# Kernel optimization log

Measured on AMD Instinct MI355X. Metric: run time of the kernel, lower is better.

Reference implementation:

```python
import jax, jax.numpy as jnp
import numpy as np

N_NODES = 65536
N_EDGES = 1048576
IN_FEATS = 128
H1 = 128
H2 = 256
N_CLASSES = 16


def setup_inputs() -> dict:
    key = jax.random.key(0)
    ks = jax.random.split(key, 12)
    s = 0.05
    x = jax.random.normal(ks[0], (N_NODES, IN_FEATS), dtype=jnp.float32)
    src = jax.random.randint(ks[1], (N_EDGES,), 0, N_NODES, dtype=jnp.int32)
    dst = jax.random.randint(ks[2], (N_EDGES,), 0, N_NODES, dtype=jnp.int32)
    # SAGEConv('pool') params: fc_pool (bias), fc_self (no bias), fc_neigh (no bias), output bias
    Wp = jax.random.normal(ks[3], (H1, IN_FEATS), dtype=jnp.float32) * s
    bp = jnp.zeros((H1,), dtype=jnp.float32)
    Ws = jax.random.normal(ks[4], (H1, IN_FEATS), dtype=jnp.float32) * s
    Wn = jax.random.normal(ks[5], (H1, H1), dtype=jnp.float32) * s
    bn = jnp.zeros((H1,), dtype=jnp.float32)
    # MLP head
    W1 = jax.random.normal(ks[6], (H2, H1), dtype=jnp.float32) * s
    b1 = jnp.zeros((H2,), dtype=jnp.float32)
    W2 = jax.random.normal(ks[7], (N_CLASSES, H2), dtype=jnp.float32) * s
    b2 = jnp.zeros((N_CLASSES,), dtype=jnp.float32)
    return {"x": x, "Wp": Wp, "bp": bp, "Ws": Ws, "Wn": Wn, "bn": bn,
            "W1": W1, "b1": b1, "W2": W2, "b2": b2, "src": src, "dst": dst}


def reference(x, Wp, bp, Ws, Wn, bn, W1, b1, W2, b2, src, dst):
    N = x.shape[0]
    # SAGEConv 'pool': per-edge MLP on gathered source features, segment-max over dst
    m = jax.nn.relu(x[src] @ Wp.T + bp)              # [E, H1]
    pooled = jax.ops.segment_max(m, dst, num_segments=N)  # [N, H1], -inf for isolated
    pooled = jnp.where(jnp.isneginf(pooled), 0.0, pooled)
    h = x @ Ws.T + pooled @ Wn.T + bn                # combine self + neigh
    h = jax.nn.leaky_relu(h)                         # slope 0.01 matches torch default
    h = jax.nn.leaky_relu(h @ W1.T + b1)
    # dropout is identity in eval mode
    h = jax.nn.sigmoid(h @ W2.T + b2)
    return h
```

## Files before the change

### kernel.cpp

```cpp
#include <hip/hip_runtime.h>
#include <cstdint>
#include <cstddef>

typedef __attribute__((ext_vector_type(8))) __bf16 bf16x8;
typedef __attribute__((ext_vector_type(4))) float f32x4;

union bf8pack { unsigned short u[8]; bf16x8 v; uint4 q; };

static __device__ __forceinline__ unsigned short f2b(float f) {
    union { float f; unsigned int u; } v; v.f = f;
    unsigned int u = v.u;
    unsigned int r = (u + 0x7fffu + ((u >> 16) & 1u)) >> 16;
    return (unsigned short)r;
}

template<int K, int ACT>
__global__ __launch_bounds__(256) void mfma_gemm(
    const unsigned short* __restrict__ A, int strideA,
    const unsigned short* __restrict__ W,
    const float* __restrict__ bias,
    unsigned short* __restrict__ C, int Ncols)
{
    const int nt = Ncols >> 7;
    const int bm = (int)blockIdx.x / nt, bn = (int)blockIdx.x % nt;
    const int w  = threadIdx.x >> 6;
    const int wm = w & 1, wn = w >> 1;
    const int l  = threadIdx.x & 63;
    const int lr = l & 15, quad = l >> 4;
    const int m0 = bm * 128 + wm * 64;
    const int n0 = bn * 128 + wn * 64;

    f32x4 acc[4][4];
#pragma unroll
    for (int i = 0; i < 4; i++)
#pragma unroll
        for (int j = 0; j < 4; j++) acc[i][j] = (f32x4){0.f, 0.f, 0.f, 0.f};

    const unsigned short* Ap = A + (size_t)(m0 + lr) * strideA + quad * 8;
    const unsigned short* Bp = W + (size_t)(n0 + lr) * K + quad * 8;

    for (int ks = 0; ks < K / 32; ks++) {
        bf16x8 af[4], bf[4];
#pragma unroll
        for (int i = 0; i < 4; i++)
            af[i] = *(const bf16x8*)(Ap + (size_t)i * 16 * strideA + ks * 32);
#pragma unroll
        for (int i = 0; i < 4; i++)
            bf[i] = *(const bf16x8*)(Bp + (size_t)i * 16 * K + ks * 32);
#pragma unroll
        for (int mi = 0; mi < 4; mi++)
#pragma unroll
            for (int ni = 0; ni < 4; ni++)
                acc[mi][ni] = __builtin_amdgcn_mfma_f32_16x16x32_bf16(
                    af[mi], bf[ni], acc[mi][ni], 0, 0, 0);
    }

#pragma unroll
    for (int ni = 0; ni < 4; ni++) {
        const int col = n0 + ni * 16 + lr;
        const float bv = bias[col];
#pragma unroll
        for (int mi = 0; mi < 4; mi++) {
#pragma unroll
            for (int r = 0; r < 4; r++) {
                const int row = m0 + mi * 16 + quad * 4 + r;
                float v = acc[mi][ni][r] + bv;
                if (ACT == 1) v = v > 0.f ? v : 0.f;
                if (ACT == 2) v = v > 0.f ? v : 0.01f * v;
                C[(size_t)row * Ncols + col] = f2b(v);
            }
        }
    }
}

__global__ __launch_bounds__(256) void k1_fused(
    const float* __restrict__ x, const unsigned short* __restrict__ Wp_b,
    const float* __restrict__ bias, unsigned short* __restrict__ bufX,
    unsigned short* __restrict__ y)
{
    const int bm = blockIdx.x;
    const int w  = threadIdx.x >> 6;
    const int wm = w & 1, wn = w >> 1;
    const int l  = threadIdx.x & 63;
    const int lr = l & 15, quad = l >> 4;
    const int m0 = bm * 128 + wm * 64;
    const int n0 = wn * 64;

    f32x4 acc[4][4];
#pragma unroll
    for (int i = 0; i < 4; i++)
#pragma unroll
        for (int j = 0; j < 4; j++) acc[i][j] = (f32x4){0.f, 0.f, 0.f, 0.f};

    const float* Ap = x + (size_t)(m0 + lr) * 128 + quad * 8;
    const unsigned short* Bp = Wp_b + (size_t)(n0 + lr) * 128 + quad * 8;

#pragma unroll
    for (int ks = 0; ks < 4; ks++) {
        bf16x8 af[4], bf[4];
#pragma unroll
        for (int i = 0; i < 4; i++) {
            const float* p = Ap + (size_t)i * 16 * 128 + ks * 32;
            float4 f0 = *(const float4*)p;
            float4 f1 = *(const float4*)(p + 4);
            bf8pack pk;
            pk.u[0] = f2b(f0.x); pk.u[1] = f2b(f0.y);
            pk.u[2] = f2b(f0.z); pk.u[3] = f2b(f0.w);
            pk.u[4] = f2b(f1.x); pk.u[5] = f2b(f1.y);
            pk.u[6] = f2b(f1.z); pk.u[7] = f2b(f1.w);
            af[i] = pk.v;
            if (wn == 0)
                *(uint4*)(bufX + (size_t)(m0 + lr + i * 16) * 256 + ks * 32 + quad * 8) = pk.q;
        }
#pragma unroll
        for (int i = 0; i < 4; i++)
            bf[i] = *(const bf16x8*)(Bp + (size_t)i * 16 * 128 + ks * 32);
#pragma unroll
        for (int mi = 0; mi < 4; mi++)
#pragma unroll
            for (int ni = 0; ni < 4; ni++)
                acc[mi][ni] = __builtin_amdgcn_mfma_f32_16x16x32_bf16(
                    af[mi], bf[ni], acc[mi][ni], 0, 0, 0);
    }

#pragma unroll
    for (int ni = 0; ni < 4; ni++) {
        const int col = n0 + ni * 16 + lr;
        const float bv = bias[col];
#pragma unroll
        for (int mi = 0; mi < 4; mi++) {
#pragma unroll
            for (int r = 0; r < 4; r++) {
                const int row = m0 + mi * 16 + quad * 4 + r;
                float v = acc[mi][ni][r] + bv;
                v = v > 0.f ? v : 0.f;
                y[(size_t)row * 128 + col] = f2b(v);
            }
        }
    }
}

__global__ __launch_bounds__(256) void head_mfma(
    const unsigned short* __restrict__ H, const unsigned short* __restrict__ W2b,
    const float* __restrict__ b2, float* __restrict__ out)
{
    const int wave = (int)(blockIdx.x * 4) + (threadIdx.x >> 6);
    const int l = threadIdx.x & 63;
    const int lr = l & 15, quad = l >> 4;
    const int m0 = wave * 16;
    f32x4 acc = (f32x4){0.f, 0.f, 0.f, 0.f};
#pragma unroll
    for (int ks = 0; ks < 8; ks++) {
        bf16x8 a = *(const bf16x8*)(H + (size_t)(m0 + lr) * 256 + ks * 32 + quad * 8);
        bf16x8 b = *(const bf16x8*)(W2b + (size_t)lr * 256 + ks * 32 + quad * 8);
        acc = __builtin_amdgcn_mfma_f32_16x16x32_bf16(a, b, acc, 0, 0, 0);
    }
    const float bv = b2[lr];
#pragma unroll
    for (int r = 0; r < 4; r++) {
        const int row = m0 + quad * 4 + r;
        float v = acc[r] + bv;
        out[(size_t)row * 16 + lr] = 1.f / (1.f + __expf(-v));
    }
}

__global__ __launch_bounds__(256) void count_conv(
    const int* __restrict__ dst, int* __restrict__ bcnt, int E, int ebks,
    const float* __restrict__ Wp, const float* __restrict__ Ws,
    const float* __restrict__ Wn, const float* __restrict__ W1,
    const float* __restrict__ W2,
    unsigned short* __restrict__ Wp_b, unsigned short* __restrict__ Wcat,
    unsigned short* __restrict__ W1_b, unsigned short* __restrict__ W2_b)
{
    if ((int)blockIdx.x >= ebks) {
        int i = ((int)blockIdx.x - ebks) * 256 + threadIdx.x;
        if (i < 16384) {
            Wp_b[i] = f2b(Wp[i]);
        } else if (i < 49152) {
            int j = i - 16384; int o = j >> 8, k = j & 255;
            Wcat[j] = f2b(k < 128 ? Ws[o * 128 + k] : Wn[o * 128 + (k - 128)]);
        } else if (i < 81920) {
            W1_b[i - 49152] = f2b(W1[i - 49152]);
        } else if (i < 86016) {
            W2_b[i - 81920] = f2b(W2[i - 81920]);
        }
        return;
    }
    __shared__ int h[2048];
    for (int i = threadIdx.x; i < 2048; i += 256) h[i] = 0;
    __syncthreads();
    int base = blockIdx.x * 4096;
#pragma unroll
    for (int i = 0; i < 16; i++) {
        int e = base + i * 256 + threadIdx.x;
        if (e < E) atomicAdd(&h[((unsigned)dst[e]) >> 5], 1);
    }
    __syncthreads();
    for (int i = threadIdx.x; i < 2048; i += 256)
        if (h[i]) atomicAdd(&bcnt[i], h[i]);
}

__global__ __launch_bounds__(1024) void bucket_scan(
    const int* __restrict__ bcnt, int* __restrict__ boff, int* __restrict__ bcur)
{
    __shared__ int s[1024];
    int t = threadIdx.x;
    int c0 = bcnt[2 * t], c1 = bcnt[2 * t + 1];
    s[t] = c0 + c1;
    __syncthreads();
    for (int d = 1; d < 1024; d <<= 1) {
        int add = (t >= d) ? s[t - d] : 0;
        __syncthreads();
        s[t] += add;
        __syncthreads();
    }
    int ex = (t == 0) ? 0 : s[t - 1];
    boff[2 * t] = ex;          bcur[2 * t] = ex;
    boff[2 * t + 1] = ex + c0; bcur[2 * t + 1] = ex + c0;
    if (t == 1023) boff[2048] = s[1023];
}

__global__ __launch_bounds__(256) void bucket_scatter(
    const int* __restrict__ src, const int* __restrict__ dst,
    int* __restrict__ bcur, unsigned int* __restrict__ pairs, int E)
{
    __shared__ int h[2048];
    __shared__ int base_l[2048];
    __shared__ int cnt[2048];
    for (int i = threadIdx.x; i < 2048; i += 256) { h[i] = 0; cnt[i] = 0; }
    __syncthreads();
    int base = blockIdx.x * 4096;
    int d_r[16], s_r[16];
#pragma unroll
    for (int i = 0; i < 16; i++) {
        int e = base + i * 256 + threadIdx.x;
        if (e < E) {
            d_r[i] = dst[e]; s_r[i] = src[e];
            atomicAdd(&h[((unsigned)d_r[i]) >> 5], 1);
        } else d_r[i] = -1;
    }
    __syncthreads();
    for (int i = threadIdx.x; i < 2048; i += 256)
        base_l[i] = h[i] ? atomicAdd(&bcur[i], h[i]) : 0;
    __syncthreads();
#pragma unroll
    for (int i = 0; i < 16; i++) {
        if (d_r[i] >= 0) {
            int b = ((unsigned)d_r[i]) >> 5;
            int pos = base_l[b] + atomicAdd(&cnt[b], 1);
            pairs[pos] = ((unsigned)s_r[i] << 5) | ((unsigned)d_r[i] & 31u);
        }
    }
}

__global__ __launch_bounds__(256) void bucket_pool3(
    const unsigned int* __restrict__ yu, const int* __restrict__ boff,
    const unsigned int* __restrict__ pairs, unsigned short* __restrict__ bufX)
{
    __shared__ unsigned short ldsSrc[2048];
    __shared__ int bin[32], offl[32], cnt2[32];
    const int b = blockIdx.x;
    const int tid = threadIdx.x;
    if (tid < 32) { bin[tid] = 0; cnt2[tid] = 0; }
    __syncthreads();
    const int beg = boff[b];
    const int nb = boff[b + 1] - beg;

    for (int i = tid; i < nb; i += 256)
        atomicAdd(&bin[pairs[beg + i] & 31u], 1);
    __syncthreads();
    if (tid == 0) {
        int run = 0;
        for (int i = 0; i < 32; i++) { offl[i] = run; run += bin[i]; }
    }
    __syncthreads();
    for (int i = tid; i < nb; i += 256) {
        unsigned int p = pairs[beg + i];
        int d = p & 31u;
        int slot = offl[d] + atomicAdd(&cnt2[d], 1);
        ldsSrc[slot] = (unsigned short)(p >> 5);
    }
    __syncthreads();

    const int w = tid >> 6, lane = tid & 63;
    for (int ni = 0; ni < 8; ni++) {
        const int n = w * 8 + ni;
        const int e0 = offl[n], cnt = bin[n];
        float ax = 0.f, ay = 0.f;
        for (int e = 0; e < cnt; e += 8) {
            int s[8]; unsigned int v[8];
#pragma unroll
            for (int j = 0; j < 8; j++) {
                int idx = e + j; idx = idx < cnt ? idx : cnt - 1;
                s[j] = ldsSrc[e0 + idx];
            }
#pragma unroll
            for (int j = 0; j < 8; j++) v[j] = yu[(size_t)s[j] * 64 + lane];
#pragma unroll
            for (int j = 0; j < 8; j++) {
                ax = fmaxf(ax, __uint_as_float(v[j] << 16));
                ay = fmaxf(ay, __uint_as_float(v[j] & 0xffff0000u));
            }
        }
        unsigned int packed = (__float_as_uint(ax) >> 16) | (__float_as_uint(ay) & 0xffff0000u);
        ((unsigned int*)bufX)[(size_t)(b * 32 + n) * 128 + 64 + lane] = packed;
    }
}

extern "C" void kernel_launch(void* const* d_in, const int* in_sizes, int n_in,
                              void* d_out, int out_size, void* d_ws, size_t ws_size,
                              hipStream_t stream)
{
    const float* x  = (const float*)d_in[0];
    const float* Wp = (const float*)d_in[1];
    const float* bp = (const float*)d_in[2];
    const float* Ws = (const float*)d_in[3];
    const float* Wn = (const float*)d_in[4];
    const float* bn = (const float*)d_in[5];
    const float* W1 = (const float*)d_in[6];
    const float* b1 = (const float*)d_in[7];
    const float* W2 = (const float*)d_in[8];
    const float* b2 = (const float*)d_in[9];
    const int* src  = (const int*)d_in[10];
    const int* dst  = (const int*)d_in[11];
    float* out = (float*)d_out;

    const int N = in_sizes[0] / 128;
    const int E = in_sizes[10];

    unsigned short* bufX = (unsigned short*)d_ws;
    unsigned short* y    = (unsigned short*)((char*)d_ws + (size_t)32 * 1024 * 1024);
    unsigned short* hbuf = (unsigned short*)((char*)d_ws + (size_t)48 * 1024 * 1024);
    unsigned short* h2   = (unsigned short*)((char*)d_ws + (size_t)64 * 1024 * 1024);

    unsigned short* Wp_b = (unsigned short*)((char*)d_ws + (size_t)96 * 1024 * 1024);
    unsigned short* Wcat = Wp_b + 16384;
    unsigned short* W1_b = Wcat + 32768;
    unsigned short* W2_b = W1_b + 32768;
    int* bcnt = (int*)(W2_b + 4096);
    int* boff = bcnt + 2048;
    int* bcur = boff + 2049 + 3;
    unsigned int* pairs = (unsigned int*)(bcur + 2048);

    dim3 blk(256);
    const int ebks = (E + 4095) / 4096;
    const int cbks = (86016 + 255) / 256;

    hipMemsetAsync(bcnt, 0, 2048 * sizeof(int), stream);
    count_conv<<<ebks + cbks, blk, 0, stream>>>(
        dst, bcnt, E, ebks, Wp, Ws, Wn, W1, W2, Wp_b, Wcat, W1_b, W2_b);
    bucket_scan<<<1, 1024, 0, stream>>>(bcnt, boff, bcur);
    bucket_scatter<<<ebks, blk, 0, stream>>>(src, dst, bcur, pairs, E);

    k1_fused<<<N / 128, blk, 0, stream>>>(x, Wp_b, bp, bufX, y);

    bucket_pool3<<<2048, blk, 0, stream>>>((const unsigned int*)y, boff, pairs, bufX);

    mfma_gemm<256, 2><<<(N / 128) * 1, blk, 0, stream>>>(
        bufX, 256, Wcat, bn, hbuf, 128);

    mfma_gemm<128, 2><<<(N / 128) * 2, blk, 0, stream>>>(
        hbuf, 128, W1_b, b1, h2, 256);

    head_mfma<<<N / 64, blk, 0, stream>>>(h2, W2_b, b2, out);
}
```

Measured before the change: 243.1 us.

## Fuse all GNN stages into one cooperative persistent kernel with grid syncs

Replaces the chain of separate kernel launches (count, scan, scatter, pool, GEMMs, head) with a single cooperative persistent kernel that loops over work items and separates stages with grid.sync. It also overlaps the dst histogram and weight conversion with the first pool-MLP GEMM using an atomic tile cursor, and converts Wp to bf16 inline instead of precomputing it. The goal is to cut per-launch overhead and inter-kernel gaps. In exchange it adds grid-wide barriers, caps the grid at 512 blocks, and hardcodes the problem sizes, dropping the edge-count bounds checks. A multi-kernel fallback is kept for when the cooperative launch fails.

```diff
diff --git a/kernel.cpp b/kernel.cpp
--- a/kernel.cpp
+++ b/kernel.cpp
@@ -1,6 +1,9 @@
 #include <hip/hip_runtime.h>
+#include <hip/hip_cooperative_groups.h>
 #include <cstdint>
 #include <cstddef>
+
+namespace cg = cooperative_groups;
 
 typedef __attribute__((ext_vector_type(8))) __bf16 bf16x8;
 typedef __attribute__((ext_vector_type(4))) float f32x4;
@@ -14,21 +17,17 @@
     return (unsigned short)r;
 }
 
+
 template<int K, int ACT>
-__global__ __launch_bounds__(256) void mfma_gemm(
+static __device__ __forceinline__ void gemm_tile(
     const unsigned short* __restrict__ A, int strideA,
-    const unsigned short* __restrict__ W,
-    const float* __restrict__ bias,
-    unsigned short* __restrict__ C, int Ncols)
-{
-    const int nt = Ncols >> 7;
-    const int bm = (int)blockIdx.x / nt, bn = (int)blockIdx.x % nt;
-    const int w  = threadIdx.x >> 6;
-    const int wm = w & 1, wn = w >> 1;
-    const int l  = threadIdx.x & 63;
-    const int lr = l & 15, quad = l >> 4;
+    const unsigned short* __restrict__ W, const float* __restrict__ bias,
+    unsigned short* __restrict__ C, int Ncols, int bm, int bnt, int tid)
+{
+    const int w = tid >> 6, wm = w & 1, wn = w >> 1;
+    const int l = tid & 63, lr = l & 15, quad = l >> 4;
     const int m0 = bm * 128 + wm * 64;
-    const int n0 = bn * 128 + wn * 64;
+    const int n0 = bnt * 128 + wn * 64;
 
     f32x4 acc[4][4];
 #pragma unroll
@@ -39,20 +38,21 @@
     const unsigned short* Ap = A + (size_t)(m0 + lr) * strideA + quad * 8;
     const unsigned short* Bp = W + (size_t)(n0 + lr) * K + quad * 8;
 
+#pragma unroll
     for (int ks = 0; ks < K / 32; ks++) {
-        bf16x8 af[4], bf[4];
+        bf16x8 af[4], bfr[4];
 #pragma unroll
         for (int i = 0; i < 4; i++)
             af[i] = *(const bf16x8*)(Ap + (size_t)i * 16 * strideA + ks * 32);
 #pragma unroll
         for (int i = 0; i < 4; i++)
-            bf[i] = *(const bf16x8*)(Bp + (size_t)i * 16 * K + ks * 32);
+            bfr[i] = *(const bf16x8*)(Bp + (size_t)i * 16 * K + ks * 32);
 #pragma unroll
         for (int mi = 0; mi < 4; mi++)
 #pragma unroll
             for (int ni = 0; ni < 4; ni++)
                 acc[mi][ni] = __builtin_amdgcn_mfma_f32_16x16x32_bf16(
-                    af[mi], bf[ni], acc[mi][ni], 0, 0, 0);
+                    af[mi], bfr[ni], acc[mi][ni], 0, 0, 0);
     }
 
 #pragma unroll
@@ -73,16 +73,13 @@
     }
 }
 
-__global__ __launch_bounds__(256) void k1_fused(
-    const float* __restrict__ x, const unsigned short* __restrict__ Wp_b,
-    const float* __restrict__ bias, unsigned short* __restrict__ bufX,
-    unsigned short* __restrict__ y)
-{
-    const int bm = blockIdx.x;
-    const int w  = threadIdx.x >> 6;
-    const int wm = w & 1, wn = w >> 1;
-    const int l  = threadIdx.x & 63;
-    const int lr = l & 15, quad = l >> 4;
+static __device__ __forceinline__ void k1_tile(
+    int bm, const float* __restrict__ x, const float* __restrict__ Wp,
+    const float* __restrict__ bp, unsigned short* __restrict__ bufX,
+    unsigned short* __restrict__ yb, int tid)
+{
+    const int w = tid >> 6, wm = w & 1, wn = w >> 1;
+    const int l = tid & 63, lr = l & 15, quad = l >> 4;
     const int m0 = bm * 128 + wm * 64;
     const int n0 = wn * 64;
 
@@ -93,16 +90,15 @@
         for (int j = 0; j < 4; j++) acc[i][j] = (f32x4){0.f, 0.f, 0.f, 0.f};
 
     const float* Ap = x + (size_t)(m0 + lr) * 128 + quad * 8;
-    const unsigned short* Bp = Wp_b + (size_t)(n0 + lr) * 128 + quad * 8;
+    const float* Bp = Wp + (size_t)(n0 + lr) * 128 + quad * 8;
 
 #pragma unroll
     for (int ks = 0; ks < 4; ks++) {
-        bf16x8 af[4], bf[4];
+        bf16x8 af[4], bfr[4];
 #pragma unroll
         for (int i = 0; i < 4; i++) {
             const float* p = Ap + (size_t)i * 16 * 128 + ks * 32;
-            float4 f0 = *(const float4*)p;
-            float4 f1 = *(const float4*)(p + 4);
+            float4 f0 = *(const float4*)p, f1 = *(const float4*)(p + 4);
             bf8pack pk;
             pk.u[0] = f2b(f0.x); pk.u[1] = f2b(f0.y);
             pk.u[2] = f2b(f0.z); pk.u[3] = f2b(f0.w);
@@ -113,20 +109,28 @@
                 *(uint4*)(bufX + (size_t)(m0 + lr + i * 16) * 256 + ks * 32 + quad * 8) = pk.q;
         }
 #pragma unroll
-        for (int i = 0; i < 4; i++)
-            bf[i] = *(const bf16x8*)(Bp + (size_t)i * 16 * 128 + ks * 32);
+        for (int i = 0; i < 4; i++) {
+            const float* p = Bp + (size_t)i * 16 * 128 + ks * 32;
+            float4 f0 = *(const float4*)p, f1 = *(const float4*)(p + 4);
+            bf8pack pk;
+            pk.u[0] = f2b(f0.x); pk.u[1] = f2b(f0.y);
+            pk.u[2] = f2b(f0.z); pk.u[3] = f2b(f0.w);
+            pk.u[4] = f2b(f1.x); pk.u[5] = f2b(f1.y);
+            pk.u[6] = f2b(f1.z); pk.u[7] = f2b(f1.w);
+            bfr[i] = pk.v;
+        }
 #pragma unroll
         for (int mi = 0; mi < 4; mi++)
 #pragma unroll
             for (int ni = 0; ni < 4; ni++)
                 acc[mi][ni] = __builtin_amdgcn_mfma_f32_16x16x32_bf16(
-                    af[mi], bf[ni], acc[mi][ni], 0, 0, 0);
+                    af[mi], bfr[ni], acc[mi][ni], 0, 0, 0);
     }
 
 #pragma unroll
     for (int ni = 0; ni < 4; ni++) {
         const int col = n0 + ni * 16 + lr;
-        const float bv = bias[col];
+        const float bv = bp[col];
 #pragma unroll
         for (int mi = 0; mi < 4; mi++) {
 #pragma unroll
@@ -134,137 +138,110 @@
                 const int row = m0 + mi * 16 + quad * 4 + r;
                 float v = acc[mi][ni][r] + bv;
                 v = v > 0.f ? v : 0.f;
-                y[(size_t)row * 128 + col] = f2b(v);
+                yb[(size_t)row * 128 + col] = f2b(v);
             }
         }
     }
 }
 
-__global__ __launch_bounds__(256) void head_mfma(
-    const unsigned short* __restrict__ H, const unsigned short* __restrict__ W2b,
-    const float* __restrict__ b2, float* __restrict__ out)
-{
-    const int wave = (int)(blockIdx.x * 4) + (threadIdx.x >> 6);
-    const int l = threadIdx.x & 63;
-    const int lr = l & 15, quad = l >> 4;
-    const int m0 = wave * 16;
-    f32x4 acc = (f32x4){0.f, 0.f, 0.f, 0.f};
-#pragma unroll
-    for (int ks = 0; ks < 8; ks++) {
-        bf16x8 a = *(const bf16x8*)(H + (size_t)(m0 + lr) * 256 + ks * 32 + quad * 8);
-        bf16x8 b = *(const bf16x8*)(W2b + (size_t)lr * 256 + ks * 32 + quad * 8);
-        acc = __builtin_amdgcn_mfma_f32_16x16x32_bf16(a, b, acc, 0, 0, 0);
-    }
-    const float bv = b2[lr];
-#pragma unroll
-    for (int r = 0; r < 4; r++) {
-        const int row = m0 + quad * 4 + r;
-        float v = acc[r] + bv;
-        out[(size_t)row * 16 + lr] = 1.f / (1.f + __expf(-v));
-    }
-}
-
-__global__ __launch_bounds__(256) void count_conv(
-    const int* __restrict__ dst, int* __restrict__ bcnt, int E, int ebks,
-    const float* __restrict__ Wp, const float* __restrict__ Ws,
-    const float* __restrict__ Wn, const float* __restrict__ W1,
-    const float* __restrict__ W2,
-    unsigned short* __restrict__ Wp_b, unsigned short* __restrict__ Wcat,
-    unsigned short* __restrict__ W1_b, unsigned short* __restrict__ W2_b)
-{
-    if ((int)blockIdx.x >= ebks) {
-        int i = ((int)blockIdx.x - ebks) * 256 + threadIdx.x;
-        if (i < 16384) {
-            Wp_b[i] = f2b(Wp[i]);
-        } else if (i < 49152) {
-            int j = i - 16384; int o = j >> 8, k = j & 255;
-            Wcat[j] = f2b(k < 128 ? Ws[o * 128 + k] : Wn[o * 128 + (k - 128)]);
-        } else if (i < 81920) {
-            W1_b[i - 49152] = f2b(W1[i - 49152]);
-        } else if (i < 86016) {
-            W2_b[i - 81920] = f2b(W2[i - 81920]);
-        }
-        return;
-    }
-    __shared__ int h[2048];
-    for (int i = threadIdx.x; i < 2048; i += 256) h[i] = 0;
-    __syncthreads();
-    int base = blockIdx.x * 4096;
+static __device__ __forceinline__ void count_chunk(
+    int c, const int* __restrict__ dst, int* __restrict__ bcnt,
+    int* smem, int tid)
+{
+    int* h = smem;
+    for (int i = tid; i < 2048; i += 256) h[i] = 0;
+    __syncthreads();
+    const int base = c * 8192;
+#pragma unroll
+    for (int i = 0; i < 32; i++)
+        atomicAdd(&h[((unsigned)dst[base + i * 256 + tid]) >> 5], 1);
+    __syncthreads();
+    for (int i = tid; i < 2048; i += 256)
+        if (h[i]) atomicAdd(&bcnt[i], h[i]);
+    __syncthreads();
+}
+
+static __device__ __forceinline__ void convw_chunk(
+    int c, const float* __restrict__ Ws, const float* __restrict__ Wn,
+    const float* __restrict__ W1, const float* __restrict__ W2,
+    unsigned short* __restrict__ Wcat, unsigned short* __restrict__ W1_b,
+    unsigned short* __restrict__ W2_b, int tid)
+{
+    int i = c * 16384 + tid;
+    for (int k = 0; k < 64; k++, i += 256) {
+        if (i < 32768) {
+            int o = i >> 8, kk = i & 255;
+            Wcat[i] = f2b(kk < 128 ? Ws[o * 128 + kk] : Wn[o * 128 + (kk - 128)]);
+        } else if (i < 65536) {
+            W1_b[i - 32768] = f2b(W1[i - 32768]);
+        } else if (i < 69632) {
+            W2_b[i - 65536] = f2b(W2[i - 65536]);
+        }
+    }
+}
+
+static __device__ __forceinline__ void scan2048(
+    const int* __restrict__ bcnt, int* __restrict__ boff,
+    int* __restrict__ bcur, int* smem, int tid)
+{
+    int loc[8]; const int base = tid * 8; int s = 0;
+#pragma unroll
+    for (int j = 0; j < 8; j++) { loc[j] = bcnt[base + j]; s += loc[j]; }
+    smem[tid] = s;
+    __syncthreads();
+    for (int d = 1; d < 256; d <<= 1) {
+        int add = (tid >= d) ? smem[tid - d] : 0;
+        __syncthreads();
+        smem[tid] += add;
+        __syncthreads();
+    }
+    int run = tid ? smem[tid - 1] : 0;
+#pragma unroll
+    for (int j = 0; j < 8; j++) { boff[base + j] = run; bcur[base + j] = run; run += loc[j]; }
+    if (tid == 255) boff[2048] = run;
+    __syncthreads();
+}
+
+static __device__ __forceinline__ void scatter_chunk(
+    int c, const int* __restrict__ src, const int* __restrict__ dst,
+    int* __restrict__ bcur, unsigned int* __restrict__ pairs,
+    int* smem, int tid)
+{
+    int* h = smem; int* base_l = smem + 2048; int* cntl = smem + 4096;
+    for (int i = tid; i < 2048; i += 256) { h[i] = 0; cntl[i] = 0; }
+    __syncthreads();
+    const int base = c * 4096;
+    int d_r[16], s_r[16];
 #pragma unroll
     for (int i = 0; i < 16; i++) {
-        int e = base + i * 256 + threadIdx.x;
-        if (e < E) atomicAdd(&h[((unsigned)dst[e]) >> 5], 1);
-    }
-    __syncthreads();
-    for (int i = threadIdx.x; i < 2048; i += 256)
-        if (h[i]) atomicAdd(&bcnt[i], h[i]);
-}
-
-__global__ __launch_bounds__(1024) void bucket_scan(
-    const int* __restrict__ bcnt, int* __restrict__ boff, int* __restrict__ bcur)
-{
-    __shared__ int s[1024];
-    int t = threadIdx.x;
-    int c0 = bcnt[2 * t], c1 = bcnt[2 * t + 1];
-    s[t] = c0 + c1;
-    __syncthreads();
-    for (int d = 1; d < 1024; d <<= 1) {
-        int add = (t >= d) ? s[t - d] : 0;
-        __syncthreads();
-        s[t] += add;
-        __syncthreads();
-    }
-    int ex = (t == 0) ? 0 : s[t - 1];
-    boff[2 * t] = ex;          bcur[2 * t] = ex;
-    boff[2 * t + 1] = ex + c0; bcur[2 * t + 1] = ex + c0;
-    if (t == 1023) boff[2048] = s[1023];
-}
-
-__global__ __launch_bounds__(256) void bucket_scatter(
-    const int* __restrict__ src, const int* __restrict__ dst,
-    int* __restrict__ bcur, unsigned int* __restrict__ pairs, int E)
-{
-    __shared__ int h[2048];
-    __shared__ int base_l[2048];
-    __shared__ int cnt[2048];
-    for (int i = threadIdx.x; i < 2048; i += 256) { h[i] = 0; cnt[i] = 0; }
-    __syncthreads();
-    int base = blockIdx.x * 4096;
-    int d_r[16], s_r[16];
+        int e = base + i * 256 + tid;
+        d_r[i] = dst[e]; s_r[i] = src[e];
+        atomicAdd(&h[((unsigned)d_r[i]) >> 5], 1);
+    }
+    __syncthreads();
+    for (int i = tid; i < 2048; i += 256)
+        base_l[i] = h[i] ? atomicAdd(&bcur[i], h[i]) : 0;
+    __syncthreads();
 #pragma unroll
     for (int i = 0; i < 16; i++) {
-        int e = base + i * 256 + threadIdx.x;
-        if (e < E) {
-            d_r[i] = dst[e]; s_r[i] = src[e];
-            atomicAdd(&h[((unsigned)d_r[i]) >> 5], 1);
-        } else d_r[i] = -1;
-    }
-    __syncthreads();
-    for (int i = threadIdx.x; i < 2048; i += 256)
-        base_l[i] = h[i] ? atomicAdd(&bcur[i], h[i]) : 0;
-    __syncthreads();
-#pragma unroll
-    for (int i = 0; i < 16; i++) {
-        if (d_r[i] >= 0) {
-            int b = ((unsigned)d_r[i]) >> 5;
-            int pos = base_l[b] + atomicAdd(&cnt[b], 1);
-            pairs[pos] = ((unsigned)s_r[i] << 5) | ((unsigned)d_r[i] & 31u);
-        }
-    }
-}
-
-__global__ __launch_bounds__(256) void bucket_pool3(
-    const unsigned int* __restrict__ yu, const int* __restrict__ boff,
-    const unsigned int* __restrict__ pairs, unsigned short* __restrict__ bufX)
-{
-    __shared__ unsigned short ldsSrc[2048];
-    __shared__ int bin[32], offl[32], cnt2[32];
-    const int b = blockIdx.x;
-    const int tid = threadIdx.x;
+        int bk = ((unsigned)d_r[i]) >> 5;
+        int pos = base_l[bk] + atomicAdd(&cntl[bk], 1);
+        pairs[pos] = ((unsigned)s_r[i] << 5) | ((unsigned)d_r[i] & 31u);
+    }
+    __syncthreads();
+}
+
+static __device__ __forceinline__ void pool_bucket(
+    int bk, const unsigned int* __restrict__ yu, const int* __restrict__ boff,
+    const unsigned int* __restrict__ pairs, unsigned short* __restrict__ bufX,
+    int* smem, int tid)
+{
+    int* bin = smem; int* offl = smem + 32; int* cnt2 = smem + 64;
+    unsigned short* ldsSrc = (unsigned short*)(smem + 96);
     if (tid < 32) { bin[tid] = 0; cnt2[tid] = 0; }
     __syncthreads();
-    const int beg = boff[b];
-    const int nb = boff[b + 1] - beg;
+    const int beg = boff[bk];
+    const int nb = boff[bk + 1] - beg;
 
     for (int i = tid; i < nb; i += 256)
         atomicAdd(&bin[pairs[beg + i] & 31u], 1);
@@ -277,8 +254,7 @@
     for (int i = tid; i < nb; i += 256) {
         unsigned int p = pairs[beg + i];
         int d = p & 31u;
-        int slot = offl[d] + atomicAdd(&cnt2[d], 1);
-        ldsSrc[slot] = (unsigned short)(p >> 5);
+        ldsSrc[offl[d] + atomicAdd(&cnt2[d], 1)] = (unsigned short)(p >> 5);
     }
     __syncthreads();
 
@@ -303,8 +279,151 @@
             }
         }
         unsigned int packed = (__float_as_uint(ax) >> 16) | (__float_as_uint(ay) & 0xffff0000u);
-        ((unsigned int*)bufX)[(size_t)(b * 32 + n) * 128 + 64 + lane] = packed;
-    }
+        ((unsigned int*)bufX)[(size_t)(bk * 32 + n) * 128 + 64 + lane] = packed;
+    }
+    __syncthreads();
+}
+
+static __device__ __forceinline__ void head_job(
+    int j, const unsigned short* __restrict__ H,
+    const unsigned short* __restrict__ W2b, const float* __restrict__ b2,
+    float* __restrict__ out, int tid)
+{
+    const int w = tid >> 6, l = tid & 63, lr = l & 15, quad = l >> 4;
+    const int m0 = j * 64 + w * 16;
+    f32x4 acc = (f32x4){0.f, 0.f, 0.f, 0.f};
+#pragma unroll
+    for (int ks = 0; ks < 8; ks++) {
+        bf16x8 a = *(const bf16x8*)(H + (size_t)(m0 + lr) * 256 + ks * 32 + quad * 8);
+        bf16x8 bb = *(const bf16x8*)(W2b + (size_t)lr * 256 + ks * 32 + quad * 8);
+        acc = __builtin_amdgcn_mfma_f32_16x16x32_bf16(a, bb, acc, 0, 0, 0);
+    }
+    const float bv = b2[lr];
+#pragma unroll
+    for (int r = 0; r < 4; r++) {
+        const int row = m0 + quad * 4 + r;
+        float v = acc[r] + bv;
+        out[(size_t)row * 16 + lr] = 1.f / (1.f + __expf(-v));
+    }
+}
+
+__global__ __launch_bounds__(256, 2) void fused_gnn(
+    const float* __restrict__ x,  const float* __restrict__ Wp,
+    const float* __restrict__ bp, const float* __restrict__ Ws,
+    const float* __restrict__ Wn, const float* __restrict__ bn,
+    const float* __restrict__ W1, const float* __restrict__ b1,
+    const float* __restrict__ W2, const float* __restrict__ b2,
+    const int* __restrict__ src,  const int* __restrict__ dst,
+    float* __restrict__ out,
+    unsigned short* bufX, unsigned short* y, unsigned short* hbuf,
+    unsigned short* h2, unsigned short* Wcat, unsigned short* W1_b,
+    unsigned short* W2_b, int* bcnt, int* cursor, int* boff, int* bcur,
+    unsigned int* pairs)
+{
+    __shared__ int smem[6144];
+    __shared__ int sh_t;
+    cg::grid_group grid = cg::this_grid();
+    const int b = blockIdx.x;
+    const int G = gridDim.x;
+    const int tid = threadIdx.x;
+
+    for (int c = b; c < 128; c += G) count_chunk(c, dst, bcnt, smem, tid);
+    for (int c = b; c < 5; c += G)
+        convw_chunk(c, Ws, Wn, W1, W2, Wcat, W1_b, W2_b, tid);
+    for (;;) {
+        if (tid == 0) sh_t = atomicAdd(cursor, 1);
+        __syncthreads();
+        const int t = sh_t;
+        __syncthreads();
+        if (t >= 512) break;
+        k1_tile(t, x, Wp, bp, bufX, y, tid);
+    }
+    grid.sync();
+
+    if (b == 0) scan2048(bcnt, boff, bcur, smem, tid);
+    grid.sync();
+
+    for (int c = b; c < 256; c += G)
+        scatter_chunk(c, src, dst, bcur, pairs, smem, tid);
+    grid.sync();
+
+    for (int c = b; c < 2048; c += G)
+        pool_bucket(c, (const unsigned int*)y, boff, pairs, bufX, smem, tid);
+    grid.sync();
+
+    for (int c = b; c < 512; c += G)
+        gemm_tile<256, 2>(bufX, 256, Wcat, bn, hbuf, 128, c, 0, tid);
+    grid.sync();
+
+    for (int c = b; c < 1024; c += G)
+        gemm_tile<128, 2>(hbuf, 128, W1_b, b1, h2, 256, c >> 1, c & 1, tid);
+    grid.sync();
+
+    for (int c = b; c < 1024; c += G)
+        head_job(c, h2, W2_b, b2, out, tid);
+}
+
+__global__ __launch_bounds__(256) void fb_count_conv(
+    const int* dst, int* bcnt, const float* Ws, const float* Wn,
+    const float* W1, const float* W2, unsigned short* Wcat,
+    unsigned short* W1_b, unsigned short* W2_b)
+{
+    __shared__ int smem[2048];
+    if ((int)blockIdx.x < 128)
+        count_chunk(blockIdx.x, dst, bcnt, smem, threadIdx.x);
+    else
+        convw_chunk(blockIdx.x - 128, Ws, Wn, W1, W2, Wcat, W1_b, W2_b, threadIdx.x);
+}
+
+__global__ __launch_bounds__(256) void fb_scan(
+    const int* bcnt, int* boff, int* bcur)
+{
+    __shared__ int smem[256];
+    scan2048(bcnt, boff, bcur, smem, threadIdx.x);
+}
+
+__global__ __launch_bounds__(256) void fb_scatter(
+    const int* src, const int* dst, int* bcur, unsigned int* pairs)
+{
+    __shared__ int smem[6144];
+    scatter_chunk(blockIdx.x, src, dst, bcur, pairs, smem, threadIdx.x);
+}
+
+__global__ __launch_bounds__(256) void fb_k1(
+    const float* x, const float* Wp, const float* bp,
+    unsigned short* bufX, unsigned short* y)
+{
+    k1_tile(blockIdx.x, x, Wp, bp, bufX, y, threadIdx.x);
+}
+
+__global__ __launch_bounds__(256) void fb_pool(
+    const unsigned int* yu, const int* boff, const unsigned int* pairs,
+    unsigned short* bufX)
+{
+    __shared__ int smem[2144];
+    pool_bucket(blockIdx.x, yu, boff, pairs, bufX, smem, threadIdx.x);
+}
+
+__global__ __launch_bounds__(256) void fb_k4(
+    const unsigned short* bufX, const unsigned short* Wcat, const float* bn,
+    unsigned short* hbuf)
+{
+    gemm_tile<256, 2>(bufX, 256, Wcat, bn, hbuf, 128, blockIdx.x, 0, threadIdx.x);
+}
+
+__global__ __launch_bounds__(256) void fb_k5(
+    const unsigned short* hbuf, const unsigned short* W1_b, const float* b1,
+    unsigned short* h2)
+{
+    gemm_tile<128, 2>(hbuf, 128, W1_b, b1, h2, 256,
+                      (int)blockIdx.x >> 1, (int)blockIdx.x & 1, threadIdx.x);
+}
+
+__global__ __launch_bounds__(256) void fb_head(
+    const unsigned short* h2, const unsigned short* W2_b, const float* b2,
+    float* out)
+{
+    head_job(blockIdx.x, h2, W2_b, b2, out, threadIdx.x);
 }
 
 extern "C" void kernel_launch(void* const* d_in, const int* in_sizes, int n_in,
@@ -325,42 +444,52 @@
     const int* dst  = (const int*)d_in[11];
     float* out = (float*)d_out;
 
-    const int N = in_sizes[0] / 128;
-    const int E = in_sizes[10];
-
     unsigned short* bufX = (unsigned short*)d_ws;
     unsigned short* y    = (unsigned short*)((char*)d_ws + (size_t)32 * 1024 * 1024);
     unsigned short* hbuf = (unsigned short*)((char*)d_ws + (size_t)48 * 1024 * 1024);
     unsigned short* h2   = (unsigned short*)((char*)d_ws + (size_t)64 * 1024 * 1024);
 
-    unsigned short* Wp_b = (unsigned short*)((char*)d_ws + (size_t)96 * 1024 * 1024);
-    unsigned short* Wcat = Wp_b + 16384;
+    unsigned short* Wcat = (unsigned short*)((char*)d_ws + (size_t)96 * 1024 * 1024);
     unsigned short* W1_b = Wcat + 32768;
     unsigned short* W2_b = W1_b + 32768;
-    int* bcnt = (int*)(W2_b + 4096);
-    int* boff = bcnt + 2048;
-    int* bcur = boff + 2049 + 3;
+    int* bcnt   = (int*)(W2_b + 4096);
+    int* cursor = bcnt + 2048;
+    int* boff   = cursor + 16;
+    int* bcur   = boff + 2064;
     unsigned int* pairs = (unsigned int*)(bcur + 2048);
 
-    dim3 blk(256);
-    const int ebks = (E + 4095) / 4096;
-    const int cbks = (86016 + 255) / 256;
-
-    hipMemsetAsync(bcnt, 0, 2048 * sizeof(int), stream);
-    count_conv<<<ebks + cbks, blk, 0, stream>>>(
-        dst, bcnt, E, ebks, Wp, Ws, Wn, W1, W2, Wp_b, Wcat, W1_b, W2_b);
-    bucket_scan<<<1, 1024, 0, stream>>>(bcnt, boff, bcur);
-    bucket_scatter<<<ebks, blk, 0, stream>>>(src, dst, bcur, pairs, E);
-
-    k1_fused<<<N / 128, blk, 0, stream>>>(x, Wp_b, bp, bufX, y);
-
-    bucket_pool3<<<2048, blk, 0, stream>>>((const unsigned int*)y, boff, pairs, bufX);
-
-    mfma_gemm<256, 2><<<(N / 128) * 1, blk, 0, stream>>>(
-        bufX, 256, Wcat, bn, hbuf, 128);
-
-    mfma_gemm<128, 2><<<(N / 128) * 2, blk, 0, stream>>>(
-        hbuf, 128, W1_b, b1, h2, 256);
-
-    head_mfma<<<N / 64, blk, 0, stream>>>(h2, W2_b, b2, out);
-}
+    hipMemsetAsync(bcnt, 0, (2048 + 16) * sizeof(int), stream);
+
+    bool ok = false;
+    int maxBlk = 0;
+    hipError_t qe = hipOccupancyMaxActiveBlocksPerMultiprocessor(
+        &maxBlk, (const void*)fused_gnn, 256, 0);
+    if (qe == hipSuccess && maxBlk > 0) {
+        int gridN = maxBlk * 256;
+        if (gridN > 512) gridN = 512;
+        void* args[] = {
+            (void*)&x, (void*)&Wp, (void*)&bp, (void*)&Ws, (void*)&Wn, (void*)&bn,
+            (void*)&W1, (void*)&b1, (void*)&W2, (void*)&b2, (void*)&src, (void*)&dst,
+            (void*)&out, (void*)&bufX, (void*)&y, (void*)&hbuf, (void*)&h2,
+            (void*)&Wcat, (void*)&W1_b, (void*)&W2_b, (void*)&bcnt, (void*)&cursor,
+            (void*)&boff, (void*)&bcur, (void*)&pairs
+        };
+        hipError_t le = hipLaunchCooperativeKernel((void*)fused_gnn, dim3(gridN),
+                                                   dim3(256), args, 0, stream);
+        ok = (le == hipSuccess);
+    }
+    if (!ok) {
+        (void)hipGetLastError();
+        dim3 blk(256);
+        fb_count_conv<<<133, blk, 0, stream>>>(dst, bcnt, Ws, Wn, W1, W2,
+                                               Wcat, W1_b, W2_b);
+        fb_k1<<<512, blk, 0, stream>>>(x, Wp, bp, bufX, y);
+        fb_scan<<<1, blk, 0, stream>>>(bcnt, boff, bcur);
+        fb_scatter<<<256, blk, 0, stream>>>(src, dst, bcur, pairs);
+        fb_pool<<<2048, blk, 0, stream>>>((const unsigned int*)y, boff, pairs, bufX);
+        fb_k4<<<512, blk, 0, stream>>>(bufX, Wcat, bn, hbuf);
+        fb_k5<<<1024, blk, 0, stream>>>(hbuf, W1_b, b1, h2);
+        fb_head<<<1024, blk, 0, stream>>>(h2, W2_b, b2, out);
+    }
+    (void)in_sizes; (void)n_in; (void)out_size; (void)ws_size;
+}
```

Result: slower. 510.3 us (+109.9%).

## Fuse W1 MLP layer and classifier head into one kernel via LDS

Applied to the files above, without the earlier changes.

Merges the hidden-layer GEMM (128->256 with leaky ReLU) and the 256->16 sigmoid head into a single kernel. The intermediate activation is kept in padded shared memory instead of being written to and reread from global memory, and one launch is dropped. In exchange each block does more register-heavy MFMA work (32 accumulators per lane), reads A and B fragments straight from global memory without LDS staging, and uses about 33KB of LDS, which may lower occupancy.

```diff
diff --git a/kernel.cpp b/kernel.cpp
--- a/kernel.cpp
+++ b/kernel.cpp
@@ -140,26 +140,74 @@
     }
 }
 
-__global__ __launch_bounds__(256) void head_mfma(
-    const unsigned short* __restrict__ H, const unsigned short* __restrict__ W2b,
+__global__ __launch_bounds__(256) void k5_head(
+    const unsigned short* __restrict__ hbuf, const unsigned short* __restrict__ W1_b,
+    const float* __restrict__ b1, const unsigned short* __restrict__ W2_b,
     const float* __restrict__ b2, float* __restrict__ out)
 {
-    const int wave = (int)(blockIdx.x * 4) + (threadIdx.x >> 6);
-    const int l = threadIdx.x & 63;
+    __shared__ unsigned short H2[64 * 264];
+    const int tid = threadIdx.x;
+    const int w = tid >> 6, l = tid & 63;
     const int lr = l & 15, quad = l >> 4;
-    const int m0 = wave * 16;
-    f32x4 acc = (f32x4){0.f, 0.f, 0.f, 0.f};
+    const int wm = w & 1, wn = w >> 1;
+    const int row0 = blockIdx.x * 64;
+
+    f32x4 acc[2][8];
+#pragma unroll
+    for (int i = 0; i < 2; i++)
+#pragma unroll
+        for (int j = 0; j < 8; j++) acc[i][j] = (f32x4){0.f, 0.f, 0.f, 0.f};
+
+    const unsigned short* Ag = hbuf + (size_t)(row0 + wm * 32 + lr) * 128 + quad * 8;
+    const unsigned short* Bp = W1_b + (size_t)(wn * 128 + lr) * 128 + quad * 8;
+
+#pragma unroll
+    for (int ks = 0; ks < 4; ks++) {
+        bf16x8 af[2], bfr[8];
+#pragma unroll
+        for (int i = 0; i < 2; i++)
+            af[i] = *(const bf16x8*)(Ag + (size_t)i * 16 * 128 + ks * 32);
+#pragma unroll
+        for (int i = 0; i < 8; i++)
+            bfr[i] = *(const bf16x8*)(Bp + (size_t)i * 16 * 128 + ks * 32);
+#pragma unroll
+        for (int mi = 0; mi < 2; mi++)
+#pragma unroll
+            for (int ni = 0; ni < 8; ni++)
+                acc[mi][ni] = __builtin_amdgcn_mfma_f32_16x16x32_bf16(
+                    af[mi], bfr[ni], acc[mi][ni], 0, 0, 0);
+    }
+
+#pragma unroll
+    for (int ni = 0; ni < 8; ni++) {
+        const int col = wn * 128 + ni * 16 + lr;
+        const float bv = b1[col];
+#pragma unroll
+        for (int mi = 0; mi < 2; mi++) {
+#pragma unroll
+            for (int r = 0; r < 4; r++) {
+                const int row = wm * 32 + mi * 16 + quad * 4 + r;
+                float v = acc[mi][ni][r] + bv;
+                v = v > 0.f ? v : 0.01f * v;
+                H2[row * 264 + col] = f2b(v);
+            }
+        }
+    }
+    __syncthreads();
+
+    const int m0 = w * 16;
+    f32x4 a2 = (f32x4){0.f, 0.f, 0.f, 0.f};
 #pragma unroll
     for (int ks = 0; ks < 8; ks++) {
-        bf16x8 a = *(const bf16x8*)(H + (size_t)(m0 + lr) * 256 + ks * 32 + quad * 8);
-        bf16x8 b = *(const bf16x8*)(W2b + (size_t)lr * 256 + ks * 32 + quad * 8);
-        acc = __builtin_amdgcn_mfma_f32_16x16x32_bf16(a, b, acc, 0, 0, 0);
+        bf16x8 a = *(const bf16x8*)&H2[(m0 + lr) * 264 + ks * 32 + quad * 8];
+        bf16x8 bb = *(const bf16x8*)(W2_b + (size_t)lr * 256 + ks * 32 + quad * 8);
+        a2 = __builtin_amdgcn_mfma_f32_16x16x32_bf16(a, bb, a2, 0, 0, 0);
     }
     const float bv = b2[lr];
 #pragma unroll
     for (int r = 0; r < 4; r++) {
-        const int row = m0 + quad * 4 + r;
-        float v = acc[r] + bv;
+        const int row = row0 + m0 + quad * 4 + r;
+        float v = a2[r] + bv;
         out[(size_t)row * 16 + lr] = 1.f / (1.f + __expf(-v));
     }
 }
@@ -331,7 +379,6 @@
     unsigned short* bufX = (unsigned short*)d_ws;
     unsigned short* y    = (unsigned short*)((char*)d_ws + (size_t)32 * 1024 * 1024);
     unsigned short* hbuf = (unsigned short*)((char*)d_ws + (size_t)48 * 1024 * 1024);
-    unsigned short* h2   = (unsigned short*)((char*)d_ws + (size_t)64 * 1024 * 1024);
 
     unsigned short* Wp_b = (unsigned short*)((char*)d_ws + (size_t)96 * 1024 * 1024);
     unsigned short* Wcat = Wp_b + 16384;
@@ -359,8 +406,5 @@
     mfma_gemm<256, 2><<<(N / 128) * 1, blk, 0, stream>>>(
         bufX, 256, Wcat, bn, hbuf, 128);
 
-    mfma_gemm<128, 2><<<(N / 128) * 2, blk, 0, stream>>>(
-        hbuf, 128, W1_b, b1, h2, 256);
-
-    head_mfma<<<N / 64, blk, 0, stream>>>(h2, W2_b, b2, out);
-}
+    k5_head<<<N / 64, blk, 0, stream>>>(hbuf, W1_b, b1, W2_b, b2, out);
+}
```

New measurement: 227.2 us. 6.5% less time.
